# Kernel optimization log

Hardware: AMD Instinct MI355X
Metric: run time of the kernel (lower is better)

The kernel has to match this reference:

```python
import jax, jax.numpy as jnp
import numpy as np
from jax import lax

BN_EPS = 1e-5


def _conv(x, w, b, stride):
    # x: [N,C,H,W], w: [O,I,3,3], stride 2, padding 1
    y = lax.conv_general_dilated(
        x, w, window_strides=(stride, stride), padding=((1, 1), (1, 1)),
        dimension_numbers=('NCHW', 'OIHW', 'NCHW'))
    return y + b[None, :, None, None]


def _batchnorm(x, gamma, beta):
    # training-mode BN: batch statistics over (N,H,W)
    mean = jnp.mean(x, axis=(0, 2, 3), keepdims=True)
    var = jnp.var(x, axis=(0, 2, 3), keepdims=True)
    xn = (x - mean) * lax.rsqrt(var + BN_EPS)
    return xn * gamma[None, :, None, None] + beta[None, :, None, None]


def _maxpool2(x):
    return lax.reduce_window(x, -jnp.inf, lax.max, (1, 1, 2, 2), (1, 1, 2, 2), 'VALID')


def setup_inputs() -> dict:
    key = jax.random.key(0)
    ks = jax.random.split(key, 8)
    B, C, H, W = 128, 3, 224, 224
    x = jax.random.normal(ks[0], (B, C, H, W), dtype=jnp.float32)
    conv1_w = jax.random.normal(ks[1], (16, 3, 3, 3), dtype=jnp.float32) * (1.0 / np.sqrt(3 * 9))
    conv1_b = jnp.zeros((16,), dtype=jnp.float32)
    bn1_g = jnp.ones((16,), dtype=jnp.float32)
    bn1_b = jnp.zeros((16,), dtype=jnp.float32)
    conv2_w = jax.random.normal(ks[2], (32, 16, 3, 3), dtype=jnp.float32) * (1.0 / np.sqrt(16 * 9))
    conv2_b = jnp.zeros((32,), dtype=jnp.float32)
    bn2_g = jnp.ones((32,), dtype=jnp.float32)
    bn2_b = jnp.zeros((32,), dtype=jnp.float32)
    fc_w = jax.random.normal(ks[3], (1, 32), dtype=jnp.float32) * (1.0 / np.sqrt(32))
    fc_b = jnp.zeros((1,), dtype=jnp.float32)
    return dict(x=x, conv1_w=conv1_w, conv1_b=conv1_b, bn1_g=bn1_g, bn1_b=bn1_b,
                conv2_w=conv2_w, conv2_b=conv2_b, bn2_g=bn2_g, bn2_b=bn2_b,
                fc_w=fc_w, fc_b=fc_b)


def reference(x, conv1_w, conv1_b, bn1_g, bn1_b, conv2_w, conv2_b, bn2_g, bn2_b, fc_w, fc_b):
    h = jax.nn.relu(_batchnorm(_conv(x, conv1_w, conv1_b, 2), bn1_g, bn1_b))   # [B,16,112,112]
    h = _maxpool2(h)                                                           # [B,16,56,56]
    h = jax.nn.relu(_batchnorm(_conv(h, conv2_w, conv2_b, 2), bn2_g, bn2_b))   # [B,32,28,28]
    h = jnp.mean(h, axis=(2, 3))                                               # AdaptiveAvgPool2d((1,1)) -> [B,32]
    logits = h @ fc_w.T + fc_b                                                 # [B,1]
    # Quantum circuit: RY(theta) on all wires, CNOT chain, <Z_0>.
    # Z on the control wire commutes with every CNOT -> expval = cos(theta).
    probs = jnp.cos(logits)                                                    # [B,1]
    return jnp.concatenate((probs, 1.0 - probs), axis=-1)                      # [B,2]
```

## Files before the change

kernel.cpp:

```cpp
#include <hip/hip_runtime.h>
#include <math.h>

#define BATCH 128
#define CIN 3
#define H 224
#define W 224
#define C1 16
#define HP 56
#define WP 56
#define C2 32
#define H2 28
#define W2 28

__global__ __launch_bounds__(256) void conv1_fused_k(
    const float* __restrict__ x, const float* __restrict__ w1,
    const float* __restrict__ b1, float2* __restrict__ mm,
    float* __restrict__ s_sum, float* __restrict__ s_sq)
{
    __shared__ float red[4][8], redq[4][8];
    const int tid = threadIdx.x;
    const int t = blockIdx.x * 256 + tid;
    const int c0 = blockIdx.y * 8;
    const int n = t / 1568;
    const int r = t % 1568;
    const int phh = r / 56;
    const int pw  = r % 56;
    const int rbase = 8 * phh - 1;
    const int cbase = 4 * pw;
    const bool topok = phh > 0;
    const bool pwok  = pw > 0;

    float accA[8][4], accB[8][4];
#pragma unroll
    for (int j = 0; j < 8; ++j) {
        const float bb = b1[c0 + j];
#pragma unroll
        for (int q = 0; q < 4; ++q) { accA[j][q] = bb; accB[j][q] = bb; }
    }

#pragma unroll
    for (int ci = 0; ci < CIN; ++ci) {
        const float* img = x + (n * CIN + ci) * (H * W);
        float p[9][5];
#pragma unroll
        for (int l = 0; l < 9; ++l) {
            const int ih = max(rbase + l, 0);
            const float* rowp = img + ih * W;
            const float4 f4 = *(const float4*)(rowp + cbase);
            const float lf = rowp[max(cbase - 1, 0)];
            const bool rok = (l > 0) || topok;
            p[l][0] = (rok && pwok) ? lf : 0.0f;
            p[l][1] = rok ? f4.x : 0.0f;
            p[l][2] = rok ? f4.y : 0.0f;
            p[l][3] = rok ? f4.z : 0.0f;
            p[l][4] = rok ? f4.w : 0.0f;
        }
#pragma unroll
        for (int j = 0; j < 8; ++j) {
            const float* wc = w1 + ((c0 + j) * CIN + ci) * 9;
#pragma unroll
            for (int kh = 0; kh < 3; ++kh) {
#pragma unroll
                for (int kw = 0; kw < 3; ++kw) {
                    const float wv = wc[kh * 3 + kw];
                    accA[j][0] += wv * p[kh][kw];
                    accA[j][1] += wv * p[kh][kw + 2];
                    accA[j][2] += wv * p[kh + 2][kw];
                    accA[j][3] += wv * p[kh + 2][kw + 2];
                    accB[j][0] += wv * p[4 + kh][kw];
                    accB[j][1] += wv * p[4 + kh][kw + 2];
                    accB[j][2] += wv * p[6 + kh][kw];
                    accB[j][3] += wv * p[6 + kh][kw + 2];
                }
            }
        }
    }

#pragma unroll
    for (int j = 0; j < 8; ++j) {
        const int o = (n * C1 + c0 + j) * (HP * WP) + (2 * phh) * WP + pw;
        const float a0 = accA[j][0], a1 = accA[j][1], a2 = accA[j][2], a3 = accA[j][3];
        const float b0 = accB[j][0], b1v = accB[j][1], b2v = accB[j][2], b3 = accB[j][3];
        mm[o] = make_float2(fmaxf(fmaxf(a0, a1), fmaxf(a2, a3)),
                            fminf(fminf(a0, a1), fminf(a2, a3)));
        mm[o + WP] = make_float2(fmaxf(fmaxf(b0, b1v), fmaxf(b2v, b3)),
                                 fminf(fminf(b0, b1v), fminf(b2v, b3)));
        float s = a0 + a1 + a2 + a3 + b0 + b1v + b2v + b3;
        float q = a0 * a0 + a1 * a1 + a2 * a2 + a3 * a3
                + b0 * b0 + b1v * b1v + b2v * b2v + b3 * b3;
#pragma unroll
        for (int off = 32; off > 0; off >>= 1) {
            s += __shfl_xor(s, off);
            q += __shfl_xor(q, off);
        }
        if ((tid & 63) == 0) { red[tid >> 6][j] = s; redq[tid >> 6][j] = q; }
    }
    __syncthreads();
    if (tid < 8) {
        atomicAdd(&s_sum[c0 + tid],
                  red[0][tid] + red[1][tid] + red[2][tid] + red[3][tid]);
    } else if (tid < 16) {
        const int j = tid - 8;
        atomicAdd(&s_sq[c0 + j],
                  redq[0][j] + redq[1][j] + redq[2][j] + redq[3][j]);
    }
}

__global__ void finalize_bn_k(const float* __restrict__ s_sum,
                              const float* __restrict__ s_sq,
                              const float* __restrict__ g,
                              const float* __restrict__ beta,
                              float* __restrict__ sc, int C, float invcount)
{
    int c = threadIdx.x;
    if (c < C) {
        float mean = s_sum[c] * invcount;
        float var  = s_sq[c] * invcount - mean * mean;
        float scale = g[c] * rsqrtf(var + 1e-5f);
        sc[c]     = scale;
        sc[C + c] = beta[c] - mean * scale;
    }
}

__global__ __launch_bounds__(256) void conv2_k(
    const float2* __restrict__ mm, const float* __restrict__ sc1,
    const float* __restrict__ w2, const float* __restrict__ b2,
    float* __restrict__ y2,
    float* __restrict__ s_sum, float* __restrict__ s_sq)
{
    __shared__ float red[4][8], redq[4][8];
    const int tid = threadIdx.x;
    const int t = blockIdx.x * 256 + tid;
    const int c0 = blockIdx.y * 8;
    const int n = t / 392;
    const int r = t % 392;
    const int ohh = r / 28;
    const int ow  = r % 28;
    const int rbase = 4 * ohh - 1;
    const bool topok = ohh > 0;
    const bool owok  = ow > 0;

    float accA[8], accB[8];
#pragma unroll
    for (int c = 0; c < 8; ++c) { accA[c] = b2[c0 + c]; accB[c] = b2[c0 + c]; }

#pragma unroll 4
    for (int ci = 0; ci < C1; ++ci) {
        const float2* pl = mm + (n * C1 + ci) * (HP * WP);
        const float s1 = sc1[ci], t1 = sc1[C1 + ci];
        float v[5][3];
#pragma unroll
        for (int l = 0; l < 5; ++l) {
            const int ih = max(rbase + l, 0);
            const float2* rowp = pl + ih * WP;
            const float4 f4 = *(const float4*)(rowp + 2 * ow);
            const float2 lp = rowp[max(2 * ow - 1, 0)];
            const bool rok = (l > 0) || topok;
            const float h0 = fmaxf(0.0f, fmaxf(s1 * lp.x + t1, s1 * lp.y + t1));
            const float h1 = fmaxf(0.0f, fmaxf(s1 * f4.x + t1, s1 * f4.y + t1));
            const float h2 = fmaxf(0.0f, fmaxf(s1 * f4.z + t1, s1 * f4.w + t1));
            v[l][0] = (rok && owok) ? h0 : 0.0f;
            v[l][1] = rok ? h1 : 0.0f;
            v[l][2] = rok ? h2 : 0.0f;
        }
#pragma unroll
        for (int c = 0; c < 8; ++c) {
            const float* wc = w2 + ((c0 + c) * C1 + ci) * 9;
            float a = accA[c];
            a += wc[0] * v[0][0]; a += wc[1] * v[0][1]; a += wc[2] * v[0][2];
            a += wc[3] * v[1][0]; a += wc[4] * v[1][1]; a += wc[5] * v[1][2];
            a += wc[6] * v[2][0]; a += wc[7] * v[2][1]; a += wc[8] * v[2][2];
            accA[c] = a;
            float b = accB[c];
            b += wc[0] * v[2][0]; b += wc[1] * v[2][1]; b += wc[2] * v[2][2];
            b += wc[3] * v[3][0]; b += wc[4] * v[3][1]; b += wc[5] * v[3][2];
            b += wc[6] * v[4][0]; b += wc[7] * v[4][1]; b += wc[8] * v[4][2];
            accB[c] = b;
        }
    }

#pragma unroll
    for (int c = 0; c < 8; ++c) {
        const int o = (n * C2 + c0 + c) * (H2 * W2) + (2 * ohh) * W2 + ow;
        y2[o] = accA[c];
        y2[o + W2] = accB[c];
        float s = accA[c] + accB[c];
        float q = accA[c] * accA[c] + accB[c] * accB[c];
#pragma unroll
        for (int off = 32; off > 0; off >>= 1) {
            s += __shfl_xor(s, off);
            q += __shfl_xor(q, off);
        }
        if ((tid & 63) == 0) { red[tid >> 6][c] = s; redq[tid >> 6][c] = q; }
    }
    __syncthreads();
    if (tid < 8) {
        atomicAdd(&s_sum[c0 + tid],
                  red[0][tid] + red[1][tid] + red[2][tid] + red[3][tid]);
    } else if (tid < 16) {
        const int c = tid - 8;
        atomicAdd(&s_sq[c0 + c],
                  redq[0][c] + redq[1][c] + redq[2][c] + redq[3][c]);
    }
}

__global__ __launch_bounds__(64) void head_k(
    const float* __restrict__ y2, const float* __restrict__ sc2,
    const float* __restrict__ fcw, float* __restrict__ logit)
{
    const int b = blockIdx.x;
    const int n = b >> 5, c = b & 31;
    const int lane = threadIdx.x;
    const float s = sc2[c], t = sc2[C2 + c];
    const float* yp = y2 + (size_t)b * (H2 * W2);
    float acc = 0.0f;
    for (int p = lane; p < H2 * W2; p += 64)
        acc += fmaxf(0.0f, s * yp[p] + t);
#pragma unroll
    for (int off = 32; off > 0; off >>= 1) acc += __shfl_xor(acc, off);
    if (lane == 0)
        atomicAdd(&logit[n], acc * (1.0f / (H2 * W2)) * fcw[c]);
}

__global__ void cos_k(const float* __restrict__ logit,
                      const float* __restrict__ fcb, float* __restrict__ out)
{
    const int n = threadIdx.x;
    const float pc = cosf(logit[n] + fcb[0]);
    out[2 * n]     = pc;
    out[2 * n + 1] = 1.0f - pc;
}

extern "C" void kernel_launch(void* const* d_in, const int* in_sizes, int n_in,
                              void* d_out, int out_size, void* d_ws, size_t ws_size,
                              hipStream_t stream) {
    const float* x   = (const float*)d_in[0];
    const float* w1  = (const float*)d_in[1];
    const float* b1  = (const float*)d_in[2];
    const float* g1  = (const float*)d_in[3];
    const float* be1 = (const float*)d_in[4];
    const float* w2  = (const float*)d_in[5];
    const float* b2  = (const float*)d_in[6];
    const float* g2  = (const float*)d_in[7];
    const float* be2 = (const float*)d_in[8];
    const float* fcw = (const float*)d_in[9];
    const float* fcb = (const float*)d_in[10];
    float* out = (float*)d_out;

    float* ws = (float*)d_ws;
    float2* mm = (float2*)ws;
    float* y2 = ws + (size_t)2 * BATCH * C1 * HP * WP;
    float* stats = y2 + (size_t)BATCH * C2 * H2 * W2;
    float* s1sum = stats;
    float* s1sq  = stats + 16;
    float* s2sum = stats + 32;
    float* s2sq  = stats + 64;
    float* logit = stats + 96;
    float* sc1   = stats + 224;
    float* sc2   = stats + 256;

    hipMemsetAsync(stats, 0, 224 * sizeof(float), stream);

    conv1_fused_k<<<dim3(784, 2), 256, 0, stream>>>(x, w1, b1, mm, s1sum, s1sq);
    finalize_bn_k<<<1, 64, 0, stream>>>(s1sum, s1sq, g1, be1, sc1, C1,
                                        1.0f / (float)(BATCH * 112 * 112));
    conv2_k<<<dim3(196, 4), 256, 0, stream>>>(mm, sc1, w2, b2, y2, s2sum, s2sq);
    finalize_bn_k<<<1, 64, 0, stream>>>(s2sum, s2sq, g2, be2, sc2, C2,
                                        1.0f / (float)(BATCH * H2 * W2));
    head_k<<<BATCH * C2, 64, 0, stream>>>(y2, sc2, fcw, logit);
    cos_k<<<1, BATCH, 0, stream>>>(logit, fcb, out);
}
```

Baseline: 240.4 us.

## Fold BN finalize into consumer kernels and use one output per thread in conv2

```diff
diff --git a/kernel.cpp b/kernel.cpp
--- a/kernel.cpp
+++ b/kernel.cpp
@@ -106,24 +106,10 @@
     }
 }
 
-__global__ void finalize_bn_k(const float* __restrict__ s_sum,
-                              const float* __restrict__ s_sq,
-                              const float* __restrict__ g,
-                              const float* __restrict__ beta,
-                              float* __restrict__ sc, int C, float invcount)
-{
-    int c = threadIdx.x;
-    if (c < C) {
-        float mean = s_sum[c] * invcount;
-        float var  = s_sq[c] * invcount - mean * mean;
-        float scale = g[c] * rsqrtf(var + 1e-5f);
-        sc[c]     = scale;
-        sc[C + c] = beta[c] - mean * scale;
-    }
-}
-
 __global__ __launch_bounds__(256) void conv2_k(
-    const float2* __restrict__ mm, const float* __restrict__ sc1,
+    const float2* __restrict__ mm,
+    const float* __restrict__ s1sum, const float* __restrict__ s1sq,
+    const float* __restrict__ g1, const float* __restrict__ be1,
     const float* __restrict__ w2, const float* __restrict__ b2,
     float* __restrict__ y2,
     float* __restrict__ s_sum, float* __restrict__ s_sq)
@@ -132,60 +118,56 @@
     const int tid = threadIdx.x;
     const int t = blockIdx.x * 256 + tid;
     const int c0 = blockIdx.y * 8;
-    const int n = t / 392;
-    const int r = t % 392;
-    const int ohh = r / 28;
-    const int ow  = r % 28;
-    const int rbase = 4 * ohh - 1;
-    const bool topok = ohh > 0;
+    const int n = t / 784;
+    const int p = t % 784;
+    const int oh = p / W2, ow = p % W2;
+    const bool topok = oh > 0;
     const bool owok  = ow > 0;
-
-    float accA[8], accB[8];
-#pragma unroll
-    for (int c = 0; c < 8; ++c) { accA[c] = b2[c0 + c]; accB[c] = b2[c0 + c]; }
-
-#pragma unroll 4
+    const float inv1 = 1.0f / (float)(BATCH * 112 * 112);
+
+    float acc[8];
+#pragma unroll
+    for (int c = 0; c < 8; ++c) acc[c] = b2[c0 + c];
+
+#pragma unroll 2
     for (int ci = 0; ci < C1; ++ci) {
+        const float mean = s1sum[ci] * inv1;
+        const float var  = s1sq[ci] * inv1 - mean * mean;
+        const float s1 = g1[ci] * rsqrtf(var + 1e-5f);
+        const float t1 = be1[ci] - mean * s1;
+
         const float2* pl = mm + (n * C1 + ci) * (HP * WP);
-        const float s1 = sc1[ci], t1 = sc1[C1 + ci];
-        float v[5][3];
-#pragma unroll
-        for (int l = 0; l < 5; ++l) {
-            const int ih = max(rbase + l, 0);
+        float v[3][3];
+#pragma unroll
+        for (int kh = 0; kh < 3; ++kh) {
+            const int ih = max(2 * oh - 1 + kh, 0);
             const float2* rowp = pl + ih * WP;
             const float4 f4 = *(const float4*)(rowp + 2 * ow);
             const float2 lp = rowp[max(2 * ow - 1, 0)];
-            const bool rok = (l > 0) || topok;
+            const bool rok = (kh > 0) || topok;
             const float h0 = fmaxf(0.0f, fmaxf(s1 * lp.x + t1, s1 * lp.y + t1));
             const float h1 = fmaxf(0.0f, fmaxf(s1 * f4.x + t1, s1 * f4.y + t1));
             const float h2 = fmaxf(0.0f, fmaxf(s1 * f4.z + t1, s1 * f4.w + t1));
-            v[l][0] = (rok && owok) ? h0 : 0.0f;
-            v[l][1] = rok ? h1 : 0.0f;
-            v[l][2] = rok ? h2 : 0.0f;
+            v[kh][0] = (rok && owok) ? h0 : 0.0f;
+            v[kh][1] = rok ? h1 : 0.0f;
+            v[kh][2] = rok ? h2 : 0.0f;
         }
 #pragma unroll
         for (int c = 0; c < 8; ++c) {
             const float* wc = w2 + ((c0 + c) * C1 + ci) * 9;
-            float a = accA[c];
+            float a = acc[c];
             a += wc[0] * v[0][0]; a += wc[1] * v[0][1]; a += wc[2] * v[0][2];
             a += wc[3] * v[1][0]; a += wc[4] * v[1][1]; a += wc[5] * v[1][2];
             a += wc[6] * v[2][0]; a += wc[7] * v[2][1]; a += wc[8] * v[2][2];
-            accA[c] = a;
-            float b = accB[c];
-            b += wc[0] * v[2][0]; b += wc[1] * v[2][1]; b += wc[2] * v[2][2];
-            b += wc[3] * v[3][0]; b += wc[4] * v[3][1]; b += wc[5] * v[3][2];
-            b += wc[6] * v[4][0]; b += wc[7] * v[4][1]; b += wc[8] * v[4][2];
-            accB[c] = b;
+            acc[c] = a;
         }
     }
 
 #pragma unroll
     for (int c = 0; c < 8; ++c) {
-        const int o = (n * C2 + c0 + c) * (H2 * W2) + (2 * ohh) * W2 + ow;
-        y2[o] = accA[c];
-        y2[o + W2] = accB[c];
-        float s = accA[c] + accB[c];
-        float q = accA[c] * accA[c] + accB[c] * accB[c];
+        const float a = acc[c];
+        y2[(n * C2 + c0 + c) * (H2 * W2) + p] = a;
+        float s = a, q = a * a;
 #pragma unroll
         for (int off = 32; off > 0; off >>= 1) {
             s += __shfl_xor(s, off);
@@ -205,13 +187,19 @@
 }
 
 __global__ __launch_bounds__(64) void head_k(
-    const float* __restrict__ y2, const float* __restrict__ sc2,
+    const float* __restrict__ y2,
+    const float* __restrict__ s2sum, const float* __restrict__ s2sq,
+    const float* __restrict__ g2, const float* __restrict__ be2,
     const float* __restrict__ fcw, float* __restrict__ logit)
 {
     const int b = blockIdx.x;
     const int n = b >> 5, c = b & 31;
     const int lane = threadIdx.x;
-    const float s = sc2[c], t = sc2[C2 + c];
+    const float inv2 = 1.0f / (float)(BATCH * H2 * W2);
+    const float mean = s2sum[c] * inv2;
+    const float var  = s2sq[c] * inv2 - mean * mean;
+    const float s = g2[c] * rsqrtf(var + 1e-5f);
+    const float t = be2[c] - mean * s;
     const float* yp = y2 + (size_t)b * (H2 * W2);
     float acc = 0.0f;
     for (int p = lane; p < H2 * W2; p += 64)
@@ -256,17 +244,12 @@
     float* s2sum = stats + 32;
     float* s2sq  = stats + 64;
     float* logit = stats + 96;
-    float* sc1   = stats + 224;
-    float* sc2   = stats + 256;
 
     hipMemsetAsync(stats, 0, 224 * sizeof(float), stream);
 
     conv1_fused_k<<<dim3(784, 2), 256, 0, stream>>>(x, w1, b1, mm, s1sum, s1sq);
-    finalize_bn_k<<<1, 64, 0, stream>>>(s1sum, s1sq, g1, be1, sc1, C1,
-                                        1.0f / (float)(BATCH * 112 * 112));
-    conv2_k<<<dim3(196, 4), 256, 0, stream>>>(mm, sc1, w2, b2, y2, s2sum, s2sq);
-    finalize_bn_k<<<1, 64, 0, stream>>>(s2sum, s2sq, g2, be2, sc2, C2,
-                                        1.0f / (float)(BATCH * H2 * W2));
-    head_k<<<BATCH * C2, 64, 0, stream>>>(y2, sc2, fcw, logit);
+    conv2_k<<<dim3(392, 4), 256, 0, stream>>>(mm, s1sum, s1sq, g1, be1,
+                                              w2, b2, y2, s2sum, s2sq);
+    head_k<<<BATCH * C2, 64, 0, stream>>>(y2, s2sum, s2sq, g2, be2, fcw, logit);
     cos_k<<<1, BATCH, 0, stream>>>(logit, fcb, out);
 }
```

New measurement: 216.9 us. -9.8%, faster.
